# Performance work log

Measured on AMD Instinct MI355X. Metric: run time of the kernel, lower is better.

Reference implementation:

```python
import jax, jax.numpy as jnp
import numpy as np

BLOCK = 128  # block_size in the original module


def weight_dequant(weight, scale):
    # weight: [O, I] fp8 values (simulated float32); scale: [O//BLOCK, I//BLOCK] fp32
    O, I = weight.shape
    w = weight.reshape(O // BLOCK, BLOCK, I // BLOCK, BLOCK)
    w = w * scale[:, None, :, None]
    return w.reshape(O, I)


def setup_inputs() -> dict:
    key = jax.random.key(0)
    k1, k2, k3, k4 = jax.random.split(key, 4)
    B, S, IN, OUT = 2, 2048, 4096, 16384
    x = jax.random.normal(k1, (B, S, IN), dtype=jnp.float32)
    weight = jax.random.normal(k2, (OUT, IN), dtype=jnp.float32)
    scale = jax.random.uniform(k3, (OUT // BLOCK, IN // BLOCK), dtype=jnp.float32, minval=0.01, maxval=0.05)
    bias = jax.random.normal(k4, (OUT,), dtype=jnp.float32)
    return {"x": x, "weight": weight, "scale": scale, "bias": bias}


def reference(x, weight, scale, bias):
    # bf16 gemm_impl path: block-wise dequant of fp8 weight, then F.linear(x, W) + bias
    w = weight_dequant(weight, scale)          # [O, I]
    out = jnp.einsum('bsi,oi->bso', x, w)      # x @ W^T
    return out + bias
```

## Files before the change

kernel.cpp:

```cpp
#include <hip/hip_runtime.h>
#include <hip/hip_bf16.h>

#define M_DIM 4096
#define N_DIM 16384
#define K_DIM 4096

typedef __bf16 bf16x8 __attribute__((ext_vector_type(8)));
typedef float f32x4 __attribute__((ext_vector_type(4)));

__device__ __forceinline__ void gload16(const void* g, void* l) {
    __builtin_amdgcn_global_load_lds((__attribute__((address_space(1))) void*)g,
                                     (__attribute__((address_space(3))) void*)l, 16, 0, 0);
}

__global__ __launch_bounds__(256) void cvt_x_kernel(const float* __restrict__ x,
                                                    __hip_bfloat16* __restrict__ out,
                                                    int ngroups) {
    int i = blockIdx.x * blockDim.x + threadIdx.x;
    int stride = gridDim.x * blockDim.x;
    for (; i < ngroups; i += stride) {
        const float4* p = (const float4*)(x + (size_t)i * 8);
        float4 v0 = p[0];
        float4 v1 = p[1];
        bf16x8 r;
        r[0] = (__bf16)v0.x; r[1] = (__bf16)v0.y; r[2] = (__bf16)v0.z; r[3] = (__bf16)v0.w;
        r[4] = (__bf16)v1.x; r[5] = (__bf16)v1.y; r[6] = (__bf16)v1.z; r[7] = (__bf16)v1.w;
        *(bf16x8*)(out + (size_t)i * 8) = r;
    }
}

__global__ __launch_bounds__(256) void dequant_w_kernel(const float* __restrict__ w,
                                                        const float* __restrict__ scale,
                                                        __hip_bfloat16* __restrict__ out) {
    const int ngroups = N_DIM * (K_DIM / 8);
    int i = blockIdx.x * blockDim.x + threadIdx.x;
    int stride = gridDim.x * blockDim.x;
    for (; i < ngroups; i += stride) {
        int row = i >> 9;
        int cg  = i & 511;
        float s = scale[(row >> 7) * (K_DIM / 128) + (cg >> 4)];
        const float4* p = (const float4*)(w + (size_t)i * 8);
        float4 v0 = p[0];
        float4 v1 = p[1];
        bf16x8 r;
        r[0] = (__bf16)(v0.x * s); r[1] = (__bf16)(v0.y * s);
        r[2] = (__bf16)(v0.z * s); r[3] = (__bf16)(v0.w * s);
        r[4] = (__bf16)(v1.x * s); r[5] = (__bf16)(v1.y * s);
        r[6] = (__bf16)(v1.z * s); r[7] = (__bf16)(v1.w * s);
        *(bf16x8*)(out + (size_t)i * 8) = r;
    }
}

template <bool ST>
__device__ __forceinline__ void kstep(const __hip_bfloat16* __restrict__ pa,
                                      const __hip_bfloat16* __restrict__ pb,
                                      const __hip_bfloat16* __restrict__ aN,
                                      const __hip_bfloat16* __restrict__ bN,
                                      char* lAn, char* lBn,
                                      f32x4 (&acc)[8][4],
                                      int arow, int brow, int c0, int c1,
                                      int srow) {
    const size_t K = K_DIM;
    bf16x8 av[4], bv[4], b1[4];

    if (ST) {
        gload16(bN + (size_t)(0 * 64 + srow) * K, lBn + 0 * 8192);
        gload16(bN + (size_t)(1 * 64 + srow) * K, lBn + 1 * 8192);
        asm volatile("s_waitcnt vmcnt(4)" ::: "memory");
    } else {
        asm volatile("s_waitcnt vmcnt(0)" ::: "memory");
    }
    __builtin_amdgcn_s_barrier();
    __builtin_amdgcn_sched_barrier(0);
    #pragma unroll
    for (int i = 0; i < 4; ++i) {
        av[i] = *(const bf16x8*)(pa + arow + i * 1024 + c0);
        bv[i] = *(const bf16x8*)(pb + brow + i * 1024 + c0);
    }
    asm volatile("s_waitcnt lgkmcnt(0)" ::: "memory");
    __builtin_amdgcn_sched_barrier(0);
    __builtin_amdgcn_s_setprio(1);
    #pragma unroll
    for (int mi = 0; mi < 4; ++mi)
        #pragma unroll
        for (int ni = 0; ni < 4; ++ni)
            acc[mi][ni] = __builtin_amdgcn_mfma_f32_16x16x32_bf16(av[mi], bv[ni], acc[mi][ni], 0, 0, 0);
    __builtin_amdgcn_s_setprio(0);
    __builtin_amdgcn_sched_barrier(0);

    if (ST) {
        gload16(bN + (size_t)(2 * 64 + srow) * K, lBn + 2 * 8192);
        gload16(bN + (size_t)(3 * 64 + srow) * K, lBn + 3 * 8192);
        asm volatile("s_waitcnt vmcnt(4)" ::: "memory");
    } else {
        asm volatile("s_waitcnt vmcnt(0)" ::: "memory");
    }
    __builtin_amdgcn_s_barrier();
    __builtin_amdgcn_sched_barrier(0);
    #pragma unroll
    for (int i = 0; i < 4; ++i)
        av[i] = *(const bf16x8*)(pa + arow + 4096 + i * 1024 + c0);
    asm volatile("s_waitcnt lgkmcnt(0)" ::: "memory");
    __builtin_amdgcn_sched_barrier(0);
    __builtin_amdgcn_s_setprio(1);
    #pragma unroll
    for (int mi = 0; mi < 4; ++mi)
        #pragma unroll
        for (int ni = 0; ni < 4; ++ni)
            acc[4 + mi][ni] = __builtin_amdgcn_mfma_f32_16x16x32_bf16(av[mi], bv[ni], acc[4 + mi][ni], 0, 0, 0);
    __builtin_amdgcn_s_setprio(0);
    __builtin_amdgcn_sched_barrier(0);

    if (ST) {
        gload16(aN + (size_t)(0 * 64 + srow) * K, lAn + 0 * 8192);
        gload16(aN + (size_t)(2 * 64 + srow) * K, lAn + 2 * 8192);
    }
    __builtin_amdgcn_s_barrier();
    __builtin_amdgcn_sched_barrier(0);
    #pragma unroll
    for (int i = 0; i < 4; ++i) {
        av[i] = *(const bf16x8*)(pa + arow + i * 1024 + c1);
        b1[i] = *(const bf16x8*)(pb + brow + i * 1024 + c1);
    }
    asm volatile("s_waitcnt lgkmcnt(0)" ::: "memory");
    __builtin_amdgcn_sched_barrier(0);
    __builtin_amdgcn_s_setprio(1);
    #pragma unroll
    for (int mi = 0; mi < 4; ++mi)
        #pragma unroll
        for (int ni = 0; ni < 4; ++ni)
            acc[mi][ni] = __builtin_amdgcn_mfma_f32_16x16x32_bf16(av[mi], b1[ni], acc[mi][ni], 0, 0, 0);
    __builtin_amdgcn_s_setprio(0);
    __builtin_amdgcn_sched_barrier(0);

    if (ST) {
        gload16(aN + (size_t)(1 * 64 + srow) * K, lAn + 1 * 8192);
        gload16(aN + (size_t)(3 * 64 + srow) * K, lAn + 3 * 8192);
    }
    __builtin_amdgcn_s_barrier();
    __builtin_amdgcn_sched_barrier(0);
    #pragma unroll
    for (int i = 0; i < 4; ++i)
        av[i] = *(const bf16x8*)(pa + arow + 4096 + i * 1024 + c1);
    asm volatile("s_waitcnt lgkmcnt(0)" ::: "memory");
    __builtin_amdgcn_sched_barrier(0);
    __builtin_amdgcn_s_setprio(1);
    #pragma unroll
    for (int mi = 0; mi < 4; ++mi)
        #pragma unroll
        for (int ni = 0; ni < 4; ++ni)
            acc[4 + mi][ni] = __builtin_amdgcn_mfma_f32_16x16x32_bf16(av[mi], b1[ni], acc[4 + mi][ni], 0, 0, 0);
    __builtin_amdgcn_s_setprio(0);
    __builtin_amdgcn_sched_barrier(0);
}

__global__ __launch_bounds__(512, 2)
void gemm_bf16_kernel(const __hip_bfloat16* __restrict__ A,
                      const __hip_bfloat16* __restrict__ Bw,
                      const float* __restrict__ bias,
                      float* __restrict__ C) {
    constexpr int Mtiles = M_DIM / 256;
    constexpr int Ntiles = N_DIM / 256;
    constexpr int nwg = Mtiles * Ntiles;
    constexpr int NT = K_DIM / 64;

    int bid = blockIdx.x;
    int swz = (bid & 7) * (nwg >> 3) + (bid >> 3);
    int bm = swz % Mtiles;
    int bn = swz / Mtiles;

    __shared__ __align__(16) __hip_bfloat16 sA[2][256 * 64];
    __shared__ __align__(16) __hip_bfloat16 sB[2][256 * 64];

    const int t = threadIdx.x;
    const int l = t & 63;
    const int w = t >> 6;
    const int wm = w >> 2;
    const int wn = w & 3;

    const int lr = l & 15;
    const int lk = l >> 4;
    const int rx = (lr & 7) << 3;

    const int srow = w * 8 + (l >> 3);
    const int scol = ((l & 7) ^ (l >> 3)) << 3;

    const size_t K = K_DIM;
    const __hip_bfloat16* aB = A  + (size_t)(bm * 256) * K + scol;
    const __hip_bfloat16* bB = Bw + (size_t)(bn * 256) * K + scol;

    f32x4 acc[8][4] = {};

    const int c0 = (lk * 8) ^ rx;
    const int c1 = (32 + lk * 8) ^ rx;
    const int arow = (wm * 128 + lr) * 64;
    const int brow = (wn * 64 + lr) * 64;

    {
        char* la_ = (char*)&sA[0][0] + w * 1024;
        char* lb_ = (char*)&sB[0][0] + w * 1024;
        #pragma unroll
        for (int j = 0; j < 4; ++j) {
            gload16(aB + (size_t)(j * 64 + srow) * K, la_ + j * 8192);
            gload16(bB + (size_t)(j * 64 + srow) * K, lb_ + j * 8192);
        }
    }
    asm volatile("s_waitcnt vmcnt(0)" ::: "memory");
    __builtin_amdgcn_s_barrier();
    __builtin_amdgcn_sched_barrier(0);

    for (int kt = 0; kt + 1 < NT; ++kt) {
        const int cur = kt & 1;
        kstep<true>(&sA[cur][0], &sB[cur][0],
                    aB + (kt + 1) * 64, bB + (kt + 1) * 64,
                    (char*)&sA[cur ^ 1][0] + w * 1024,
                    (char*)&sB[cur ^ 1][0] + w * 1024,
                    acc, arow, brow, c0, c1, srow);
    }
    {
        const int cur = (NT - 1) & 1;
        kstep<false>(&sA[cur][0], &sB[cur][0], aB, bB,
                     (char*)&sA[cur ^ 1][0] + w * 1024,
                     (char*)&sB[cur ^ 1][0] + w * 1024,
                     acc, arow, brow, c0, c1, srow);
    }

    const int crow0 = bm * 256 + wm * 128;
    const int ccol0 = bn * 256 + wn * 64;
    #pragma unroll
    for (int ni = 0; ni < 4; ++ni) {
        int col = ccol0 + ni * 16 + lr;
        float bv = bias[col];
        #pragma unroll
        for (int mi = 0; mi < 8; ++mi) {
            int rbase = crow0 + mi * 16 + lk * 4;
            #pragma unroll
            for (int j = 0; j < 4; ++j) {
                C[(size_t)(rbase + j) * N_DIM + col] = acc[mi][ni][j] + bv;
            }
        }
    }
}

__global__ __launch_bounds__(256)
void gemm_fallback(const float* __restrict__ X, const float* __restrict__ W,
                   const float* __restrict__ scale, const float* __restrict__ bias,
                   float* __restrict__ C) {
    int bm = blockIdx.x % (M_DIM / 64);
    int bn = blockIdx.x / (M_DIM / 64);
    __shared__ float sA[64][33];
    __shared__ float sB[64][33];
    int t = threadIdx.x;
    int tx = t & 15, ty = t >> 4;
    float acc[4][4] = {};
    for (int kt = 0; kt < K_DIM / 32; ++kt) {
        float s = scale[(bn >> 1) * (K_DIM / 128) + (kt >> 2)];
        #pragma unroll
        for (int i = 0; i < 8; ++i) {
            int idx = t + i * 256;
            int r = idx >> 5, c = idx & 31;
            sA[r][c] = X[(size_t)(bm * 64 + r) * K_DIM + kt * 32 + c];
            sB[r][c] = W[(size_t)(bn * 64 + r) * K_DIM + kt * 32 + c] * s;
        }
        __syncthreads();
        #pragma unroll
        for (int k = 0; k < 32; ++k) {
            float a[4], b[4];
            #pragma unroll
            for (int i = 0; i < 4; ++i) a[i] = sA[ty * 4 + i][k];
            #pragma unroll
            for (int j = 0; j < 4; ++j) b[j] = sB[tx * 4 + j][k];
            #pragma unroll
            for (int i = 0; i < 4; ++i)
                #pragma unroll
                for (int j = 0; j < 4; ++j) acc[i][j] += a[i] * b[j];
        }
        __syncthreads();
    }
    #pragma unroll
    for (int i = 0; i < 4; ++i)
        #pragma unroll
        for (int j = 0; j < 4; ++j) {
            int row = bm * 64 + ty * 4 + i;
            int col = bn * 64 + tx * 4 + j;
            C[(size_t)row * N_DIM + col] = acc[i][j] + bias[col];
        }
}

extern "C" void kernel_launch(void* const* d_in, const int* in_sizes, int n_in,
                              void* d_out, int out_size, void* d_ws, size_t ws_size,
                              hipStream_t stream) {
    const float* x     = (const float*)d_in[0];
    const float* wgt   = (const float*)d_in[1];
    const float* scale = (const float*)d_in[2];
    const float* bias  = (const float*)d_in[3];
    float* out = (float*)d_out;

    const size_t need = ((size_t)M_DIM * K_DIM + (size_t)N_DIM * K_DIM) * sizeof(__hip_bfloat16);
    if (ws_size >= need) {
        __hip_bfloat16* xbf = (__hip_bfloat16*)d_ws;
        __hip_bfloat16* wbf = xbf + (size_t)M_DIM * K_DIM;
        cvt_x_kernel<<<2048, 256, 0, stream>>>(x, xbf, M_DIM * K_DIM / 8);
        dequant_w_kernel<<<4096, 256, 0, stream>>>(wgt, scale, wbf);
        gemm_bf16_kernel<<<(M_DIM / 256) * (N_DIM / 256), 512, 0, stream>>>(xbf, wbf, bias, out);
    } else {
        gemm_fallback<<<(M_DIM / 64) * (N_DIM / 64), 256, 0, stream>>>(x, wgt, scale, bias, out);
    }
}
```

Before: 806.0 us.

## Restructure GEMM k-loop prefetch schedule with staggered global-to-LDS loads

Reorganizes the double-buffered main loop so global-to-LDS loads for the next tiles are issued at different points: half of the next A tile early, the other half of A and all of the next B tile at the end of the step. The loop is unrolled by two with fixed buffer pointers, and the prologue preloads part of the second stage. Fewer barriers are used and the vmcnt waits are relaxed, aiming to overlap memory traffic with MFMA work and cut synchronization stalls. The tighter reuse of LDS buffers risks races if the barrier placement is wrong.

```diff
diff --git a/kernel.cpp b/kernel.cpp
--- a/kernel.cpp
+++ b/kernel.cpp
@@ -51,27 +51,27 @@
     }
 }
 
-template <bool ST>
+template <bool STG1, bool STG4, bool LAST>
 __device__ __forceinline__ void kstep(const __hip_bfloat16* __restrict__ pa,
                                       const __hip_bfloat16* __restrict__ pb,
-                                      const __hip_bfloat16* __restrict__ aN,
-                                      const __hip_bfloat16* __restrict__ bN,
-                                      char* lAn, char* lBn,
+                                      const __hip_bfloat16* __restrict__ gA1,
+                                      const __hip_bfloat16* __restrict__ gA2,
+                                      const __hip_bfloat16* __restrict__ gB2,
+                                      char* lAw, char* lAr, char* lBr,
                                       f32x4 (&acc)[8][4],
-                                      int arow, int brow, int c0, int c1,
-                                      int srow) {
+                                      int arow, int brow, int c0, int c1, int srow) {
     const size_t K = K_DIM;
     bf16x8 av[4], bv[4], b1[4];
 
-    if (ST) {
-        gload16(bN + (size_t)(0 * 64 + srow) * K, lBn + 0 * 8192);
-        gload16(bN + (size_t)(1 * 64 + srow) * K, lBn + 1 * 8192);
-        asm volatile("s_waitcnt vmcnt(4)" ::: "memory");
-    } else {
-        asm volatile("s_waitcnt vmcnt(0)" ::: "memory");
-    }
+    if (LAST) asm volatile("s_waitcnt vmcnt(0)" ::: "memory");
+    else      asm volatile("s_waitcnt vmcnt(6)" ::: "memory");
+    __builtin_amdgcn_sched_barrier(0);
     __builtin_amdgcn_s_barrier();
     __builtin_amdgcn_sched_barrier(0);
+    if (STG1) {
+        gload16(gA1 + (size_t)(64 + srow) * K, lAw + 8192);
+        gload16(gA1 + (size_t)(192 + srow) * K, lAw + 3 * 8192);
+    }
     #pragma unroll
     for (int i = 0; i < 4; ++i) {
         av[i] = *(const bf16x8*)(pa + arow + i * 1024 + c0);
@@ -88,18 +88,11 @@
     __builtin_amdgcn_s_setprio(0);
     __builtin_amdgcn_sched_barrier(0);
 
-    if (ST) {
-        gload16(bN + (size_t)(2 * 64 + srow) * K, lBn + 2 * 8192);
-        gload16(bN + (size_t)(3 * 64 + srow) * K, lBn + 3 * 8192);
-        asm volatile("s_waitcnt vmcnt(4)" ::: "memory");
-    } else {
-        asm volatile("s_waitcnt vmcnt(0)" ::: "memory");
-    }
-    __builtin_amdgcn_s_barrier();
-    __builtin_amdgcn_sched_barrier(0);
     #pragma unroll
     for (int i = 0; i < 4; ++i)
         av[i] = *(const bf16x8*)(pa + arow + 4096 + i * 1024 + c0);
+    __builtin_amdgcn_sched_barrier(0);
+    __builtin_amdgcn_s_barrier();
     asm volatile("s_waitcnt lgkmcnt(0)" ::: "memory");
     __builtin_amdgcn_sched_barrier(0);
     __builtin_amdgcn_s_setprio(1);
@@ -111,17 +104,13 @@
     __builtin_amdgcn_s_setprio(0);
     __builtin_amdgcn_sched_barrier(0);
 
-    if (ST) {
-        gload16(aN + (size_t)(0 * 64 + srow) * K, lAn + 0 * 8192);
-        gload16(aN + (size_t)(2 * 64 + srow) * K, lAn + 2 * 8192);
-    }
-    __builtin_amdgcn_s_barrier();
-    __builtin_amdgcn_sched_barrier(0);
     #pragma unroll
     for (int i = 0; i < 4; ++i) {
         av[i] = *(const bf16x8*)(pa + arow + i * 1024 + c1);
         b1[i] = *(const bf16x8*)(pb + brow + i * 1024 + c1);
     }
+    __builtin_amdgcn_sched_barrier(0);
+    __builtin_amdgcn_s_barrier();
     asm volatile("s_waitcnt lgkmcnt(0)" ::: "memory");
     __builtin_amdgcn_sched_barrier(0);
     __builtin_amdgcn_s_setprio(1);
@@ -133,15 +122,20 @@
     __builtin_amdgcn_s_setprio(0);
     __builtin_amdgcn_sched_barrier(0);
 
-    if (ST) {
-        gload16(aN + (size_t)(1 * 64 + srow) * K, lAn + 1 * 8192);
-        gload16(aN + (size_t)(3 * 64 + srow) * K, lAn + 3 * 8192);
-    }
-    __builtin_amdgcn_s_barrier();
-    __builtin_amdgcn_sched_barrier(0);
     #pragma unroll
     for (int i = 0; i < 4; ++i)
         av[i] = *(const bf16x8*)(pa + arow + 4096 + i * 1024 + c1);
+    __builtin_amdgcn_sched_barrier(0);
+    __builtin_amdgcn_s_barrier();
+    __builtin_amdgcn_sched_barrier(0);
+    if (STG4) {
+        gload16(gA2 + (size_t)(0 + srow) * K, lAr);
+        gload16(gA2 + (size_t)(128 + srow) * K, lAr + 2 * 8192);
+        gload16(gB2 + (size_t)(0 + srow) * K, lBr);
+        gload16(gB2 + (size_t)(64 + srow) * K, lBr + 8192);
+        gload16(gB2 + (size_t)(128 + srow) * K, lBr + 2 * 8192);
+        gload16(gB2 + (size_t)(192 + srow) * K, lBr + 3 * 8192);
+    }
     asm volatile("s_waitcnt lgkmcnt(0)" ::: "memory");
     __builtin_amdgcn_sched_barrier(0);
     __builtin_amdgcn_s_setprio(1);
@@ -196,34 +190,41 @@
     const int arow = (wm * 128 + lr) * 64;
     const int brow = (wn * 64 + lr) * 64;
 
+    char* lA0 = (char*)&sA[0][0] + w * 1024;
+    char* lB0 = (char*)&sB[0][0] + w * 1024;
+    char* lA1 = (char*)&sA[1][0] + w * 1024;
+    char* lB1 = (char*)&sB[1][0] + w * 1024;
+
     {
-        char* la_ = (char*)&sA[0][0] + w * 1024;
-        char* lb_ = (char*)&sB[0][0] + w * 1024;
         #pragma unroll
         for (int j = 0; j < 4; ++j) {
-            gload16(aB + (size_t)(j * 64 + srow) * K, la_ + j * 8192);
-            gload16(bB + (size_t)(j * 64 + srow) * K, lb_ + j * 8192);
-        }
-    }
-    asm volatile("s_waitcnt vmcnt(0)" ::: "memory");
-    __builtin_amdgcn_s_barrier();
-    __builtin_amdgcn_sched_barrier(0);
-
-    for (int kt = 0; kt + 1 < NT; ++kt) {
-        const int cur = kt & 1;
-        kstep<true>(&sA[cur][0], &sB[cur][0],
-                    aB + (kt + 1) * 64, bB + (kt + 1) * 64,
-                    (char*)&sA[cur ^ 1][0] + w * 1024,
-                    (char*)&sB[cur ^ 1][0] + w * 1024,
-                    acc, arow, brow, c0, c1, srow);
-    }
-    {
-        const int cur = (NT - 1) & 1;
-        kstep<false>(&sA[cur][0], &sB[cur][0], aB, bB,
-                     (char*)&sA[cur ^ 1][0] + w * 1024,
-                     (char*)&sB[cur ^ 1][0] + w * 1024,
-                     acc, arow, brow, c0, c1, srow);
-    }
+            gload16(aB + (size_t)(j * 64 + srow) * K, lA0 + j * 8192);
+            gload16(bB + (size_t)(j * 64 + srow) * K, lB0 + j * 8192);
+        }
+        const __hip_bfloat16* a1 = aB + 64;
+        const __hip_bfloat16* b1 = bB + 64;
+        gload16(a1 + (size_t)(0 + srow) * K, lA1);
+        gload16(a1 + (size_t)(128 + srow) * K, lA1 + 2 * 8192);
+        #pragma unroll
+        for (int j = 0; j < 4; ++j)
+            gload16(b1 + (size_t)(j * 64 + srow) * K, lB1 + j * 8192);
+    }
+
+    #pragma unroll 1
+    for (int kt = 0; kt < 62; kt += 2) {
+        kstep<true, true, false>(&sA[0][0], &sB[0][0],
+                                 aB + (kt + 1) * 64, aB + (kt + 2) * 64, bB + (kt + 2) * 64,
+                                 lA1, lA0, lB0, acc, arow, brow, c0, c1, srow);
+        kstep<true, true, false>(&sA[1][0], &sB[1][0],
+                                 aB + (kt + 2) * 64, aB + (kt + 3) * 64, bB + (kt + 3) * 64,
+                                 lA0, lA1, lB1, acc, arow, brow, c0, c1, srow);
+    }
+    kstep<true, false, false>(&sA[0][0], &sB[0][0],
+                              aB + 63 * 64, aB, bB,
+                              lA1, lA0, lB0, acc, arow, brow, c0, c1, srow);
+    kstep<false, false, true>(&sA[1][0], &sB[1][0],
+                              aB, aB, bB,
+                              lA0, lA1, lB1, acc, arow, brow, c0, c1, srow);
 
     const int crow0 = bm * 256 + wm * 128;
     const int ccol0 = bn * 256 + wn * 64;
```

Result: faster. 716.3 us (-11.1%).
